# Optimization experiments

Hardware: AMD Instinct MI355X
Metric: run time of the kernel (lower is better)

Reference implementation:

```python
import jax, jax.numpy as jnp
import numpy as np
from jax import lax

B, C, L, N = 64, 64, 8192, 3
F = L // 2 + 1  # rfft bins = 4097
HID = 2 * C     # CnnEncoder ratio=2 -> 128
K = 3           # conv kernel size


def setup_inputs() -> dict:
    key = jax.random.key(0)
    ks = jax.random.split(key, 10)
    inp = {
        "x": jax.random.normal(ks[0], (B, C, L), dtype=jnp.float32),
        # spectral filter bank: [N, C, F, 2] (real/imag stacked)
        "parameter": jax.random.normal(ks[1], (N, C, F, 2), dtype=jnp.float32),
        # reweight_R CnnEncoder params (PyTorch Conv1d layout: [out, in, k])
        "wR1": jax.random.normal(ks[2], (HID, C, K), dtype=jnp.float32) * 0.05,
        "bR1": jnp.zeros((HID,), dtype=jnp.float32),
        "wR2": jax.random.normal(ks[3], (N, HID, K), dtype=jnp.float32) * 0.05,
        "bR2": jnp.zeros((N,), dtype=jnp.float32),
        # reweight_I CnnEncoder params
        "wI1": jax.random.normal(ks[4], (HID, C, K), dtype=jnp.float32) * 0.05,
        "bI1": jnp.zeros((HID,), dtype=jnp.float32),
        "wI2": jax.random.normal(ks[5], (N, HID, K), dtype=jnp.float32) * 0.05,
        "bI2": jnp.zeros((N,), dtype=jnp.float32),
    }
    return inp


def _conv1d_same(x, w, b):
    # x: [B, Cin, L]; w: [Cout, Cin, K]; SAME padding for odd K
    pad = (w.shape[-1] - 1) // 2
    y = lax.conv_general_dilated(
        x, w, window_strides=(1,), padding=[(pad, pad)],
        dimension_numbers=("NCH", "OIH", "NCH"))
    return y + b[None, :, None]


def _cnn_encoder(x, w1, b1, w2, b2):
    # conv -> SELU -> (dropout=identity in eval) -> conv -> global avg pool -> softmax over channels
    y = jax.nn.selu(_conv1d_same(x, w1, b1))
    y = _conv1d_same(y, w2, b2)
    y = jnp.mean(y, axis=-1)          # AdaptiveAvgPool1d(1) + squeeze -> [B, N]
    return jax.nn.softmax(y, axis=1)


def reference(x, parameter, wR1, bR1, wR2, bR2, wI1, bI1, wI2, bI2):
    fx = jnp.fft.rfft(x, axis=-1, norm="ortho")          # [B, C, F] complex
    W_R = parameter[..., 0]                               # [N, C, F]
    W_I = parameter[..., 1]
    C_R = _cnn_encoder(fx.real, wR1, bR1, wR2, bR2)       # [B, N]
    C_I = _cnn_encoder(fx.imag, wI1, bI1, wI2, bI2)       # [B, N]
    Kf_R = jnp.einsum("bn,ncf->bcf", C_R, W_R)            # [B, C, F]
    Kf_I = jnp.einsum("bn,ncf->bcf", C_I, W_I)
    Kf = lax.complex(Kf_R, Kf_I)
    out = jnp.fft.irfft(fx * Kf, n=L, axis=-1, norm="ortho")  # [B, C, L]
    return out
```

## Files before the change

### kernel.cpp

```cpp
#include <hip/hip_runtime.h>
#include <math.h>

#define BB 64
#define CCH 64
#define LL 8192
#define FF 4097
#define FP 4104
#define M4 4096
#define NT 65

typedef __attribute__((ext_vector_type(8))) short short8;
typedef __attribute__((ext_vector_type(4))) float floatx4;

__device__ __forceinline__ short f2bf(float v) {
    union { float f; unsigned u; } cv; cv.f = v;
    unsigned r = (cv.u + 0x7fffu + ((cv.u >> 16) & 1u)) >> 16;
    return (short)r;
}

__device__ __forceinline__ float2 cadd(float2 a, float2 b){ return make_float2(a.x+b.x, a.y+b.y); }
__device__ __forceinline__ float2 csub(float2 a, float2 b){ return make_float2(a.x-b.x, a.y-b.y); }
__device__ __forceinline__ float2 cmul(float2 a, float2 b){ return make_float2(a.x*b.x-a.y*b.y, a.x*b.y+a.y*b.x); }
template<int SIGN> __device__ __forceinline__ float2 roti(float2 a){
    return (SIGN < 0) ? make_float2(a.y, -a.x) : make_float2(-a.y, a.x);
}
template<int SIGN>
__device__ __forceinline__ void dft4(float2& a, float2& b, float2& c, float2& d){
    float2 t0 = cadd(a,c), t1 = csub(a,c), t2 = cadd(b,d), t3 = roti<SIGN>(csub(b,d));
    a = cadd(t0,t2); b = cadd(t1,t3); c = csub(t0,t2); d = csub(t1,t3);
}

template<int SIGN>
__device__ __forceinline__ void dft16(float2 v[16]){
    const float C1 = 0.9238795325112867f, S1 = 0.3826834323650898f, R2 = 0.7071067811865476f;
    const float sg = (SIGN < 0) ? -1.0f : 1.0f;
#pragma unroll
    for (int n1 = 0; n1 < 4; ++n1) dft4<SIGN>(v[n1], v[n1+4], v[n1+8], v[n1+12]);
    const float2 W1 = make_float2( C1, sg*S1);
    const float2 W2 = make_float2( R2, sg*R2);
    const float2 W3 = make_float2( S1, sg*C1);
    const float2 W6 = make_float2(-R2, sg*R2);
    const float2 W9 = make_float2(-C1, -sg*S1);
    v[5]  = cmul(v[5],  W1); v[6]  = cmul(v[6],  W2); v[7]  = cmul(v[7],  W3);
    v[9]  = cmul(v[9],  W2); v[10] = roti<SIGN>(v[10]); v[11] = cmul(v[11], W6);
    v[13] = cmul(v[13], W3); v[14] = cmul(v[14], W6); v[15] = cmul(v[15], W9);
#pragma unroll
    for (int k2 = 0; k2 < 4; ++k2) dft4<SIGN>(v[4*k2+0], v[4*k2+1], v[4*k2+2], v[4*k2+3]);
    float2 t[16];
#pragma unroll
    for (int k = 0; k < 16; ++k) t[k] = v[4*(k & 3) + (k >> 2)];
#pragma unroll
    for (int k = 0; k < 16; ++k) v[k] = t[k];
}

__device__ __forceinline__ void twiddle_pow(float2 v[16], float ang){
    float s, c; __sincosf(ang, &s, &c);
    float2 w = make_float2(c, s), t = w;
    v[1] = cmul(v[1], t);
#pragma unroll
    for (int j = 2; j < 16; ++j){ t = cmul(t, w); v[j] = cmul(v[j], t); }
}

template<int SIGN>
__device__ __forceinline__ void fft4096_regs(float2 v[16], float2* lds, int tid){
    const float TWO_PI = 6.283185307179586f;
    const float sg = (SIGN < 0) ? -1.0f : 1.0f;
    int n1 = tid & 15, hi = tid >> 4;
    dft16<SIGN>(v);
    twiddle_pow(v, sg * TWO_PI * (float)hi * (1.0f/256.0f));
#pragma unroll
    for (int j = 0; j < 16; ++j) lds[tid + 272*j] = v[j];
    __syncthreads();
#pragma unroll
    for (int j = 0; j < 16; ++j) v[j] = lds[n1 + 16*j + 272*hi];
    __syncthreads();
    dft16<SIGN>(v);
#pragma unroll
    for (int j = 0; j < 16; ++j) lds[(j*16 + hi)*17 + n1] = v[j];
    __syncthreads();
#pragma unroll
    for (int j = 0; j < 16; ++j) v[j] = lds[tid*17 + j];
    twiddle_pow(v, sg * TWO_PI * (float)tid * (1.0f/4096.0f));
    dft16<SIGN>(v);
    __syncthreads();
}

#define COSJ_INIT { 1.0f, 0.980785280403230f, 0.923879532511287f, 0.831469612302545f, \
    0.707106781186548f, 0.555570233019602f, 0.382683432365090f, 0.195090322016128f, \
    0.0f, -0.195090322016128f, -0.382683432365090f, -0.555570233019602f, \
    -0.707106781186548f, -0.831469612302545f, -0.923879532511287f, -0.980785280403230f }
#define SINJ_INIT { 0.0f, 0.195090322016128f, 0.382683432365090f, 0.555570233019602f, \
    0.707106781186548f, 0.831469612302545f, 0.923879532511287f, 0.980785280403230f, \
    1.0f, 0.980785280403230f, 0.923879532511287f, 0.831469612302545f, \
    0.707106781186548f, 0.555570233019602f, 0.382683432365090f, 0.195090322016128f }

__global__ __launch_bounds__(256, 4) void k_rfft(const float* __restrict__ x,
                                                 float* __restrict__ fxr,
                                                 float* __restrict__ fxi)
{
    __shared__ float2 lds[4352];
    int bc = blockIdx.x, tid = threadIdx.x;
    const float2* xr = (const float2*)(x + (size_t)bc * LL);
    float2 v[16];
#pragma unroll
    for (int j = 0; j < 16; ++j) v[j] = xr[tid + 256*j];
    fft4096_regs<-1>(v, lds, tid);
#pragma unroll
    for (int j = 0; j < 16; ++j) lds[tid + 256*j] = v[j];
    __syncthreads();

    const float scale = 0.011048543456039806f;
    const float COSJ[16] = COSJ_INIT;
    const float SINJ[16] = SINJ_INIT;
    size_t row = (size_t)bc * FP;
    float sA, cA; __sincosf(3.14159265358979f * (float)tid * (1.0f/4096.0f), &sA, &cA);
#pragma unroll
    for (int j = 0; j < 16; ++j){
        int k = tid + 256*j;
        if (k == 0){
            float2 z0 = lds[0];
            fxr[row + 0]  = (z0.x + z0.y) * scale; fxi[row + 0]  = 0.0f;
            fxr[row + M4] = (z0.x - z0.y) * scale; fxi[row + M4] = 0.0f;
        } else {
            float2 zk = lds[k], zm = lds[(4096 - k) & 4095];
            float er = 0.5f*(zk.x + zm.x), ei = 0.5f*(zk.y - zm.y);
            float dr = 0.5f*(zk.x - zm.x), di = 0.5f*(zk.y + zm.y);
            float cp = cA*COSJ[j] - sA*SINJ[j];
            float sp = sA*COSJ[j] + cA*SINJ[j];
            fxr[row + k] = (er + cp*di - sp*dr) * scale;
            fxi[row + k] = (ei - cp*dr - sp*di) * scale;
        }
    }
}

__global__ __launch_bounds__(256) void k_pack(const float* __restrict__ wR1,
                                              const float* __restrict__ wI1,
                                              short* __restrict__ Wp)
{
    int idx = blockIdx.x * 256 + threadIdx.x;
    if (idx >= 2 * 128 * 192) return;
    int enc = idx / (128 * 192);
    int rem = idx - enc * (128 * 192);
    int h = rem / 192;
    int k = rem - h * 192;
    int s = k >> 5;
    int j = k & 31;
    int kap = s >> 1;
    int c = (s & 1) * 32 + j;
    const float* w = enc ? wI1 : wR1;
    Wp[idx] = f2bf(w[(h * 64 + c) * 3 + kap]);
}

__global__ __launch_bounds__(256) void k_conv_mfma(const float* __restrict__ fxr,
                                                   const float* __restrict__ fxi,
                                                   const short* __restrict__ Wp,
                                                   const float* __restrict__ bR1,
                                                   const float* __restrict__ bI1,
                                                   float* __restrict__ part,
                                                   float* __restrict__ e0,
                                                   float* __restrict__ e1)
{
    __shared__ short Xt[66 * 72];
    int tile = blockIdx.x;
    int b    = blockIdx.y;
    int enc  = blockIdx.z;
    const float* src = enc ? fxi : fxr;
    const float* b1  = enc ? bI1 : bR1;
    int tid = threadIdx.x;
    int t0 = tile * 64;

    const float* xb = src + (size_t)b * 64 * FP;
    for (int ii = tid; ii < 66 * 64; ii += 256) {
        int c  = ii / 66;
        int tt = ii - c * 66;
        int tg = t0 - 1 + tt;
        float v = (tg >= 0 && tg < FF) ? xb[(size_t)c * FP + tg] : 0.0f;
        Xt[tt * 72 + c] = f2bf(v);
    }
    __syncthreads();

    int w = tid >> 6;
    int lane = tid & 63;
    int n = lane & 15;
    int q = lane >> 4;
    int h0 = w * 32;

    short8 afrag[2][6];
    const short* wbase = Wp + (size_t)enc * 128 * 192;
#pragma unroll
    for (int hb = 0; hb < 2; ++hb)
#pragma unroll
        for (int s = 0; s < 6; ++s)
            afrag[hb][s] = *(const short8*)(wbase + (h0 + hb * 16 + n) * 192 + s * 32 + q * 8);

    floatx4 acc[2][4] = {};
#pragma unroll
    for (int s = 0; s < 6; ++s) {
        int kap = s >> 1;
        int c0 = (s & 1) * 32;
#pragma unroll
        for (int tb = 0; tb < 4; ++tb) {
            short8 bfrag = *(const short8*)(&Xt[(tb * 16 + n + kap) * 72 + c0 + q * 8]);
            acc[0][tb] = __builtin_amdgcn_mfma_f32_16x16x32_bf16(afrag[0][s], bfrag, acc[0][tb], 0, 0, 0);
            acc[1][tb] = __builtin_amdgcn_mfma_f32_16x16x32_bf16(afrag[1][s], bfrag, acc[1][tb], 0, 0, 0);
        }
    }

    const float SELU_S = 1.0507009873554805f;
    const float SELU_A = 1.6732632423543772f;
    int ebase = (enc * 64 + b) * 128;
#pragma unroll
    for (int hb = 0; hb < 2; ++hb) {
        float hsum[4] = {0.0f, 0.0f, 0.0f, 0.0f};
#pragma unroll
        for (int tb = 0; tb < 4; ++tb) {
            int t = t0 + tb * 16 + n;
            bool valid = (t < FF);
#pragma unroll
            for (int r = 0; r < 4; ++r) {
                int h = h0 + hb * 16 + q * 4 + r;
                float val = acc[hb][tb][r] + b1[h];
                float y = SELU_S * (val > 0.0f ? val : SELU_A * (__expf(val) - 1.0f));
                y = valid ? y : 0.0f;
                hsum[r] += y;
                if (valid && t == 0)      e0[ebase + h] = y;
                if (valid && t == FF - 1) e1[ebase + h] = y;
            }
        }
#pragma unroll
        for (int off = 1; off < 16; off <<= 1) {
#pragma unroll
            for (int r = 0; r < 4; ++r)
                hsum[r] += __shfl_xor(hsum[r], off, 64);
        }
        if (n == 0) {
#pragma unroll
            for (int r = 0; r < 4; ++r) {
                int h = h0 + hb * 16 + q * 4 + r;
                part[((size_t)(enc * 64 + b) * 128 + h) * NT + tile] = hsum[r];
            }
        }
    }
}

__global__ __launch_bounds__(128) void k_head(const float* __restrict__ part,
                                              const float* __restrict__ e0,
                                              const float* __restrict__ e1,
                                              const float* __restrict__ wR2,
                                              const float* __restrict__ bR2,
                                              const float* __restrict__ wI2,
                                              const float* __restrict__ bI2,
                                              float* __restrict__ Cw)
{
    __shared__ float red[3][128];
    int b   = blockIdx.x;
    int enc = blockIdx.y;
    const float* w2 = enc ? wI2 : wR2;
    const float* b2 = enc ? bI2 : bR2;
    int h = threadIdx.x;
    size_t pb = ((size_t)(enc * 64 + b) * 128 + h) * NT;
    float T = 0.0f;
    for (int t = 0; t < NT; ++t) T += part[pb + t];
    float e0v = e0[(enc * 64 + b) * 128 + h];
    float e1v = e1[(enc * 64 + b) * 128 + h];
#pragma unroll
    for (int n = 0; n < 3; ++n) {
        const float* wp = w2 + (n * 128 + h) * 3;
        red[n][h] = wp[0] * (T - e1v) + wp[1] * T + wp[2] * (T - e0v);
    }
    __syncthreads();
    if (h == 0) {
        float lg[3];
        for (int n = 0; n < 3; ++n) {
            float s = 0.0f;
            for (int q = 0; q < 128; ++q) s += red[n][q];
            lg[n] = b2[n] + s / 4097.0f;
        }
        float mx = fmaxf(lg[0], fmaxf(lg[1], lg[2]));
        float ex0 = __expf(lg[0] - mx);
        float ex1 = __expf(lg[1] - mx);
        float ex2 = __expf(lg[2] - mx);
        float den = ex0 + ex1 + ex2;
        Cw[(enc * 64 + b) * 3 + 0] = ex0 / den;
        Cw[(enc * 64 + b) * 3 + 1] = ex1 / den;
        Cw[(enc * 64 + b) * 3 + 2] = ex2 / den;
    }
}

__global__ __launch_bounds__(256, 4) void k_irfft(const float* __restrict__ fxr,
                                                  const float* __restrict__ fxi,
                                                  const float* __restrict__ param,
                                                  const float* __restrict__ Cw,
                                                  float* __restrict__ out)
{
    __shared__ float2 lds[4352];
    int bc = blockIdx.x, b = bc >> 6, c = bc & 63, tid = threadIdx.x;
    float cr0 = Cw[b*3+0], cr1 = Cw[b*3+1], cr2 = Cw[b*3+2];
    float ci0 = Cw[192 + b*3+0], ci1 = Cw[192 + b*3+1], ci2 = Cw[192 + b*3+2];
    size_t row = (size_t)bc * FP;
    const float2* W0 = (const float2*)param + (size_t)(0*64 + c) * FF;
    const float2* W1 = (const float2*)param + (size_t)(1*64 + c) * FF;
    const float2* W2 = (const float2*)param + (size_t)(2*64 + c) * FF;

    for (int f = tid; f <= 4096; f += 256) {
        float2 w0 = W0[f], w1 = W1[f], w2 = W2[f];
        float kr = cr0*w0.x + cr1*w1.x + cr2*w2.x;
        float ki = ci0*w0.y + ci1*w1.y + ci2*w2.y;
        float fr = fxr[row + f], fi = fxi[row + f];
        lds[f] = make_float2(fr*kr - fi*ki, fr*ki + fi*kr);
    }
    __syncthreads();

    const float COSJ[16] = COSJ_INIT;
    const float SINJ[16] = SINJ_INIT;
    float2 v[16];
    float sA, cA; __sincosf(3.14159265358979f * (float)tid * (1.0f/4096.0f), &sA, &cA);
#pragma unroll
    for (int j = 0; j < 16; ++j) {
        int m = tid + 256*j;
        if (m == 0) {
            float p0 = lds[0].x, pn = lds[4096].x;
            v[j] = make_float2(0.5f*(p0 + pn), 0.5f*(p0 - pn));
        } else {
            float2 p = lds[m], q = lds[4096 - m];
            float er = 0.5f*(p.x + q.x), ei = 0.5f*(p.y - q.y);
            float dr = 0.5f*(p.x - q.x), di = 0.5f*(p.y + q.y);
            float cp = cA*COSJ[j] - sA*SINJ[j];
            float sp = sA*COSJ[j] + cA*SINJ[j];
            float zor = dr*cp - di*sp;
            float zoi = dr*sp + di*cp;
            v[j] = make_float2(er - zoi, ei + zor);
        }
    }
    __syncthreads();
    fft4096_regs<1>(v, lds, tid);

    const float S = 0.02209708691207961f;
    float2* orow = (float2*)(out + (size_t)bc * LL);
#pragma unroll
    for (int j = 0; j < 16; ++j) {
        float2 z = v[j];
        orow[tid + 256*j] = make_float2(S*z.x, S*z.y);
    }
}

extern "C" void kernel_launch(void* const* d_in, const int* in_sizes, int n_in,
                              void* d_out, int out_size, void* d_ws, size_t ws_size,
                              hipStream_t stream)
{
    (void)in_sizes; (void)n_in; (void)out_size; (void)ws_size;
    const float* x   = (const float*)d_in[0];
    const float* prm = (const float*)d_in[1];
    const float* wR1 = (const float*)d_in[2];
    const float* bR1 = (const float*)d_in[3];
    const float* wR2 = (const float*)d_in[4];
    const float* bR2 = (const float*)d_in[5];
    const float* wI1 = (const float*)d_in[6];
    const float* bI1 = (const float*)d_in[7];
    const float* wI2 = (const float*)d_in[8];
    const float* bI2 = (const float*)d_in[9];
    float* out = (float*)d_out;
    float* ws  = (float*)d_ws;

    size_t o = 0;
    float* fxr  = ws + o; o += (size_t)BB * CCH * FP;
    float* fxi  = ws + o; o += (size_t)BB * CCH * FP;
    float* part = ws + o; o += (size_t)2 * 64 * 128 * NT;
    float* e0   = ws + o; o += 2 * 64 * 128;
    float* e1   = ws + o; o += 2 * 64 * 128;
    float* Cw   = ws + o; o += 2 * 64 * 4;
    short* Wp   = (short*)(ws + o); o += (size_t)2 * 128 * 192 / 2;

    k_rfft<<<dim3(4096), dim3(256), 0, stream>>>(x, fxr, fxi);
    k_pack<<<dim3((2 * 128 * 192 + 255) / 256), dim3(256), 0, stream>>>(wR1, wI1, Wp);
    k_conv_mfma<<<dim3(NT, 64, 2), dim3(256), 0, stream>>>(fxr, fxi, Wp, bR1, bI1,
                                                           part, e0, e1);
    k_head<<<dim3(64, 2), dim3(128), 0, stream>>>(part, e0, e1, wR2, bR2, wI2, bI2, Cw);
    k_irfft<<<dim3(4096), dim3(256), 0, stream>>>(fxr, fxi, prm, Cw, out);
}
```

Baseline: 418.0 us.

## Persistent multi-tile conv blocks with double-buffered swizzled LDS staging

```diff
diff --git a/kernel.cpp b/kernel.cpp
--- a/kernel.cpp
+++ b/kernel.cpp
@@ -7,7 +7,8 @@
 #define FF 4097
 #define FP 4104
 #define M4 4096
-#define NT 65
+#define NCH 13
+#define TPB 5
 
 typedef __attribute__((ext_vector_type(8))) short short8;
 typedef __attribute__((ext_vector_type(4))) float floatx4;
@@ -151,33 +152,71 @@
     Wp[idx] = f2bf(w[(h * 64 + c) * 3 + kap]);
 }
 
-__global__ __launch_bounds__(256) void k_conv_mfma(const float* __restrict__ fxr,
-                                                   const float* __restrict__ fxi,
-                                                   const short* __restrict__ Wp,
-                                                   const float* __restrict__ bR1,
-                                                   const float* __restrict__ bI1,
-                                                   float* __restrict__ part,
-                                                   float* __restrict__ e0,
-                                                   float* __restrict__ e1)
-{
-    __shared__ short Xt[66 * 72];
-    int tile = blockIdx.x;
-    int b    = blockIdx.y;
-    int enc  = blockIdx.z;
+struct Stage {
+    float4 f[4];
+    float hv;
+};
+
+__device__ __forceinline__ void stage_issue(const float* __restrict__ srow,
+                                            const float* __restrict__ xb,
+                                            int tid, int hcc, int hhal,
+                                            int t0, Stage& S)
+{
+#pragma unroll
+    for (int v = 0; v < 4; ++v)
+        S.f[v] = *(const float4*)(srow + t0 + v * 4);
+    if (tid < 128) {
+        int ht  = hhal ? (t0 + 64) : (t0 - 1);
+        int hts = ht < 0 ? 0 : ht;
+        S.hv = xb[(size_t)hcc * FP + hts];
+    }
+}
+
+__device__ __forceinline__ void stage_commit(const Stage& S, short* __restrict__ Xb,
+                                             int tid, int sc, int siq, int hcc, int hhal,
+                                             int t0)
+{
+    bool allv = (t0 + 64) <= FF;
+    const float* fp = (const float*)&S.f[0];
+#pragma unroll
+    for (int u = 0; u < 16; ++u) {
+        int tloc = siq * 16 + u;
+        float val = fp[u];
+        if (!allv) val = (t0 + tloc) < FF ? val : 0.0f;
+        int tt = tloc + 1;
+        Xb[(tt * 64 + sc) ^ ((tt & 7) << 3)] = f2bf(val);
+    }
+    if (tid < 128) {
+        int ht = hhal ? (t0 + 64) : (t0 - 1);
+        float v = (ht >= 0 && ht < FF) ? S.hv : 0.0f;
+        int tt = hhal ? 65 : 0;
+        Xb[(tt * 64 + hcc) ^ ((tt & 7) << 3)] = f2bf(v);
+    }
+}
+
+__global__ __launch_bounds__(256, 3) void k_conv_mfma(const float* __restrict__ fxr,
+                                                      const float* __restrict__ fxi,
+                                                      const short* __restrict__ Wp,
+                                                      const float* __restrict__ bR1,
+                                                      const float* __restrict__ bI1,
+                                                      float* __restrict__ part,
+                                                      float* __restrict__ e0,
+                                                      float* __restrict__ e1)
+{
+    __shared__ short Xt[2][66 * 64];
+    int chunk = blockIdx.x;
+    int b     = blockIdx.y;
+    int enc   = blockIdx.z;
     const float* src = enc ? fxi : fxr;
     const float* b1  = enc ? bI1 : bR1;
     int tid = threadIdx.x;
-    int t0 = tile * 64;
-
     const float* xb = src + (size_t)b * 64 * FP;
-    for (int ii = tid; ii < 66 * 64; ii += 256) {
-        int c  = ii / 66;
-        int tt = ii - c * 66;
-        int tg = t0 - 1 + tt;
-        float v = (tg >= 0 && tg < FF) ? xb[(size_t)c * FP + tg] : 0.0f;
-        Xt[tt * 72 + c] = f2bf(v);
-    }
-    __syncthreads();
+
+    int sc   = tid >> 2;
+    int siq  = tid & 3;
+    const float* srow = xb + (size_t)sc * FP + siq * 16;
+    int hcc  = tid >> 1;
+    int hhal = tid & 1;
 
     int w = tid >> 6;
     int lane = tid & 63;
@@ -193,52 +232,91 @@
         for (int s = 0; s < 6; ++s)
             afrag[hb][s] = *(const short8*)(wbase + (h0 + hb * 16 + n) * 192 + s * 32 + q * 8);
 
-    floatx4 acc[2][4] = {};
-#pragma unroll
-    for (int s = 0; s < 6; ++s) {
-        int kap = s >> 1;
-        int c0 = (s & 1) * 32;
-#pragma unroll
-        for (int tb = 0; tb < 4; ++tb) {
-            short8 bfrag = *(const short8*)(&Xt[(tb * 16 + n + kap) * 72 + c0 + q * 8]);
-            acc[0][tb] = __builtin_amdgcn_mfma_f32_16x16x32_bf16(afrag[0][s], bfrag, acc[0][tb], 0, 0, 0);
-            acc[1][tb] = __builtin_amdgcn_mfma_f32_16x16x32_bf16(afrag[1][s], bfrag, acc[1][tb], 0, 0, 0);
-        }
-    }
+    float b1v[2][4];
+#pragma unroll
+    for (int hb = 0; hb < 2; ++hb)
+#pragma unroll
+        for (int r = 0; r < 4; ++r)
+            b1v[hb][r] = b1[h0 + hb * 16 + q * 4 + r];
 
     const float SELU_S = 1.0507009873554805f;
     const float SELU_A = 1.6732632423543772f;
     int ebase = (enc * 64 + b) * 128;
-#pragma unroll
-    for (int hb = 0; hb < 2; ++hb) {
-        float hsum[4] = {0.0f, 0.0f, 0.0f, 0.0f};
-#pragma unroll
-        for (int tb = 0; tb < 4; ++tb) {
-            int t = t0 + tb * 16 + n;
-            bool valid = (t < FF);
-#pragma unroll
-            for (int r = 0; r < 4; ++r) {
-                int h = h0 + hb * 16 + q * 4 + r;
-                float val = acc[hb][tb][r] + b1[h];
-                float y = SELU_S * (val > 0.0f ? val : SELU_A * (__expf(val) - 1.0f));
-                y = valid ? y : 0.0f;
-                hsum[r] += y;
-                if (valid && t == 0)      e0[ebase + h] = y;
-                if (valid && t == FF - 1) e1[ebase + h] = y;
+    int tbase = chunk * (TPB * 64);
+
+    {
+        Stage S0;
+        stage_issue(srow, xb, tid, hcc, hhal, tbase, S0);
+        stage_commit(S0, Xt[0], tid, sc, siq, hcc, hhal, tbase);
+    }
+    __syncthreads();
+
+    float hsum[2][4] = {{0.f,0.f,0.f,0.f},{0.f,0.f,0.f,0.f}};
+
+#pragma unroll
+    for (int ti = 0; ti < TPB; ++ti) {
+        int t0 = tbase + ti * 64;
+        const short* Xc = Xt[ti & 1];
+
+        Stage Sn;
+        if (ti + 1 < TPB)
+            stage_issue(srow, xb, tid, hcc, hhal, t0 + 64, Sn);
+
+        floatx4 acc[2][4] = {};
+#pragma unroll
+        for (int s = 0; s < 6; ++s) {
+            int kap = s >> 1;
+            int cbase = (s & 1) * 32 + q * 8;
+#pragma unroll
+            for (int tb = 0; tb < 4; ++tb) {
+                int row = tb * 16 + n + kap;
+                short8 bfrag = *(const short8*)(Xc + ((row * 64 + cbase) ^ ((row & 7) << 3)));
+                acc[0][tb] = __builtin_amdgcn_mfma_f32_16x16x32_bf16(afrag[0][s], bfrag, acc[0][tb], 0, 0, 0);
+                acc[1][tb] = __builtin_amdgcn_mfma_f32_16x16x32_bf16(afrag[1][s], bfrag, acc[1][tb], 0, 0, 0);
             }
         }
-#pragma unroll
-        for (int off = 1; off < 16; off <<= 1) {
+
+        bool edge = (t0 == 0) || (t0 == 4096);
+        bool allv = (t0 + 63) < FF;
+#pragma unroll
+        for (int hb = 0; hb < 2; ++hb) {
+#pragma unroll
+            for (int tb = 0; tb < 4; ++tb) {
+                int t = t0 + tb * 16 + n;
+                bool valid = t < FF;
+#pragma unroll
+                for (int r = 0; r < 4; ++r) {
+                    float val = acc[hb][tb][r] + b1v[hb][r];
+                    float y = SELU_S * (val > 0.0f ? val : SELU_A * (__expf(val) - 1.0f));
+                    if (!allv) y = valid ? y : 0.0f;
+                    hsum[hb][r] += y;
+                    if (edge) {
+                        int h = h0 + hb * 16 + q * 4 + r;
+                        if (t == 0)      e0[ebase + h] = y;
+                        if (t == FF - 1) e1[ebase + h] = y;
+                    }
+                }
+            }
+        }
+
+        if (ti + 1 < TPB)
+            stage_commit(Sn, Xt[(ti + 1) & 1], tid, sc, siq, hcc, hhal, t0 + 64);
+        __syncthreads();
+    }
+
+#pragma unroll
+    for (int off = 1; off < 16; off <<= 1)
+#pragma unroll
+        for (int hb = 0; hb < 2; ++hb)
 #pragma unroll
             for (int r = 0; r < 4; ++r)
-                hsum[r] += __shfl_xor(hsum[r], off, 64);
-        }
-        if (n == 0) {
-#pragma unroll
-            for (int r = 0; r < 4; ++r) {
-                int h = h0 + hb * 16 + q * 4 + r;
-                part[((size_t)(enc * 64 + b) * 128 + h) * NT + tile] = hsum[r];
-            }
+                hsum[hb][r] += __shfl_xor(hsum[hb][r], off, 64);
+
+    if (n == 0) {
+#pragma unroll
+        for (int hb = 0; hb < 2; ++hb) {
+            size_t idx = ((size_t)(chunk * 2 + enc) * 64 + b) * 128 + h0 + hb * 16 + q * 4;
+            *(float4*)(part + idx) = make_float4(hsum[hb][0], hsum[hb][1], hsum[hb][2], hsum[hb][3]);
         }
     }
 }
@@ -258,23 +336,23 @@
     const float* w2 = enc ? wI2 : wR2;
     const float* b2 = enc ? bI2 : bR2;
     int h = threadIdx.x;
-    size_t pb = ((size_t)(enc * 64 + b) * 128 + h) * NT;
     float T = 0.0f;
-    for (int t = 0; t < NT; ++t) T += part[pb + t];
+    for (int t = 0; t < NCH; ++t)
+        T += part[((size_t)(t * 2 + enc) * 64 + b) * 128 + h];
     float e0v = e0[(enc * 64 + b) * 128 + h];
     float e1v = e1[(enc * 64 + b) * 128 + h];
 #pragma unroll
-    for (int n = 0; n < 3; ++n) {
-        const float* wp = w2 + (n * 128 + h) * 3;
-        red[n][h] = wp[0] * (T - e1v) + wp[1] * T + wp[2] * (T - e0v);
+    for (int nn = 0; nn < 3; ++nn) {
+        const float* wp = w2 + (nn * 128 + h) * 3;
+        red[nn][h] = wp[0] * (T - e1v) + wp[1] * T + wp[2] * (T - e0v);
     }
     __syncthreads();
     if (h == 0) {
         float lg[3];
-        for (int n = 0; n < 3; ++n) {
+        for (int nn = 0; nn < 3; ++nn) {
             float s = 0.0f;
-            for (int q = 0; q < 128; ++q) s += red[n][q];
-            lg[n] = b2[n] + s / 4097.0f;
+            for (int qq = 0; qq < 128; ++qq) s += red[nn][qq];
+            lg[nn] = b2[nn] + s / 4097.0f;
         }
         float mx = fmaxf(lg[0], fmaxf(lg[1], lg[2]));
         float ex0 = __expf(lg[0] - mx);
@@ -322,9 +400,9 @@
             float p0 = lds[0].x, pn = lds[4096].x;
             v[j] = make_float2(0.5f*(p0 + pn), 0.5f*(p0 - pn));
         } else {
-            float2 p = lds[m], q = lds[4096 - m];
-            float er = 0.5f*(p.x + q.x), ei = 0.5f*(p.y - q.y);
-            float dr = 0.5f*(p.x - q.x), di = 0.5f*(p.y + q.y);
+            float2 p = lds[m], qq = lds[4096 - m];
+            float er = 0.5f*(p.x + qq.x), ei = 0.5f*(p.y - qq.y);
+            float dr = 0.5f*(p.x - qq.x), di = 0.5f*(p.y + qq.y);
             float cp = cA*COSJ[j] - sA*SINJ[j];
             float sp = sA*COSJ[j] + cA*SINJ[j];
             float zor = dr*cp - di*sp;
@@ -365,7 +443,7 @@
     size_t o = 0;
     float* fxr  = ws + o; o += (size_t)BB * CCH * FP;
     float* fxi  = ws + o; o += (size_t)BB * CCH * FP;
-    float* part = ws + o; o += (size_t)2 * 64 * 128 * NT;
+    float* part = ws + o; o += (size_t)NCH * 2 * 64 * 128;
     float* e0   = ws + o; o += 2 * 64 * 128;
     float* e1   = ws + o; o += 2 * 64 * 128;
     float* Cw   = ws + o; o += 2 * 64 * 4;
@@ -373,8 +451,8 @@
 
     k_rfft<<<dim3(4096), dim3(256), 0, stream>>>(x, fxr, fxi);
     k_pack<<<dim3((2 * 128 * 192 + 255) / 256), dim3(256), 0, stream>>>(wR1, wI1, Wp);
-    k_conv_mfma<<<dim3(NT, 64, 2), dim3(256), 0, stream>>>(fxr, fxi, Wp, bR1, bI1,
-                                                           part, e0, e1);
+    k_conv_mfma<<<dim3(NCH, 64, 2), dim3(256), 0, stream>>>(fxr, fxi, Wp, bR1, bI1,
+                                                            part, e0, e1);
     k_head<<<dim3(64, 2), dim3(128), 0, stream>>>(part, e0, e1, wR2, bR2, wI2, bI2, Cw);
     k_irfft<<<dim3(4096), dim3(256), 0, stream>>>(fxr, fxi, prm, Cw, out);
 }
```

New measurement: 489.2 us. +17.0%, slower.
